# Performance work log

Measured on AMD Instinct MI355X. Metric: run time of the kernel, lower is better.

The kernel has to match this reference:

```python
import jax, jax.numpy as jnp
import numpy as np

TEMPERATURE = 0.07
TOP_MARGIN = 0.95
BOTTOM_MARGIN = 0.05

BATCH = 8192
DIM = 1024


def setup_inputs() -> dict:
    key = jax.random.key(0)
    kA, kB = jax.random.split(key)
    embedding_A = jax.random.normal(kA, (BATCH, DIM), dtype=jnp.float32)
    embedding_B = jax.random.normal(kB, (BATCH, DIM), dtype=jnp.float32)
    return {"embedding_A": embedding_A, "embedding_B": embedding_B}


def _l2norm(x):
    return x * jax.lax.rsqrt(jnp.sum(x * x, axis=-1, keepdims=True))


def reference(embedding_A, embedding_B):
    a = _l2norm(embedding_A)
    b = _l2norm(embedding_B)
    B = a.shape[0]
    sim = a @ b.T                                   # [B, B]
    pos = jnp.diagonal(sim)                         # [B]
    eye = jnp.eye(B, dtype=bool)
    upper = pos[:, None] * TOP_MARGIN
    lower = pos[:, None] * BOTTOM_MARGIN
    neg_mask = (sim <= upper) & (sim >= lower) & ~eye   # [B, B]

    # Per-row CE over [positive, hard negatives] == masked logsumexp - pos/tau.
    z = sim / TEMPERATURE
    full_mask = neg_mask | eye                      # positive always included
    masked = jnp.where(full_mask, z, -jnp.inf)
    m = jnp.max(masked, axis=1, keepdims=True)      # finite: diag always present
    lse = m[:, 0] + jnp.log(jnp.sum(jnp.exp(masked - m), axis=1))
    per_row = lse - pos / TEMPERATURE               # [B]

    valid = jnp.any(neg_mask, axis=1)               # rows with >=1 negative
    count = jnp.sum(valid)
    total = jnp.sum(jnp.where(valid, per_row, 0.0))
    return total / jnp.maximum(count, 1).astype(total.dtype)
```

## Files before the change

### kernel.cpp

```cpp
#include <hip/hip_runtime.h>
#include <hip/hip_bf16.h>

#define BATCH 8192
#define DIM   1024
#define INV_TAU (1.0f / 0.07f)
#define TOPM 0.95f
#define BOTM 0.05f

#define BM 256
#define BN 256
#define BK 64
#define NT (DIM / BK)

typedef __attribute__((ext_vector_type(4))) float f32x4;
typedef __attribute__((ext_vector_type(8))) short bf16x8;

typedef __attribute__((address_space(3))) void       lds_void_t;
typedef const __attribute__((address_space(1))) void gbl_void_t;

__device__ inline void async_copy16(const void* g, void* l) {
    __builtin_amdgcn_global_load_lds((gbl_void_t*)g, (lds_void_t*)l, 16, 0, 0);
}

__device__ inline unsigned short f2bf(float f) {
    __hip_bfloat16 h = __float2bfloat16(f);
    return *reinterpret_cast<unsigned short*>(&h);
}

__global__ __launch_bounds__(256) void prep_kernel(
    const float* __restrict__ A, const float* __restrict__ B,
    unsigned short* __restrict__ An, unsigned short* __restrict__ Bn,
    float* __restrict__ pos, float* __restrict__ S)
{
    int row = blockIdx.x;
    int t = threadIdx.x;
    const float4* a4 = (const float4*)(A + (size_t)row * DIM);
    const float4* b4 = (const float4*)(B + (size_t)row * DIM);
    float4 av = a4[t];
    float4 bv = b4[t];
    float sa = av.x*av.x + av.y*av.y + av.z*av.z + av.w*av.w;
    float sb = bv.x*bv.x + bv.y*bv.y + bv.z*bv.z + bv.w*bv.w;
    float dp = av.x*bv.x + av.y*bv.y + av.z*bv.z + av.w*bv.w;
    #pragma unroll
    for (int d = 32; d > 0; d >>= 1) {
        sa += __shfl_down(sa, d);
        sb += __shfl_down(sb, d);
        dp += __shfl_down(dp, d);
    }
    __shared__ float red[3][4];
    int lane = t & 63, w = t >> 6;
    if (lane == 0) { red[0][w] = sa; red[1][w] = sb; red[2][w] = dp; }
    __syncthreads();
    sa = red[0][0] + red[0][1] + red[0][2] + red[0][3];
    sb = red[1][0] + red[1][1] + red[1][2] + red[1][3];
    dp = red[2][0] + red[2][1] + red[2][2] + red[2][3];
    float ra = rsqrtf(sa);
    float rb = rsqrtf(sb);
    if (t == 0) {
        pos[row] = dp * ra * rb;
        S[row] = 0.0f;
    }
    ushort4 oa, ob;
    oa.x = f2bf(av.x * ra); oa.y = f2bf(av.y * ra);
    oa.z = f2bf(av.z * ra); oa.w = f2bf(av.w * ra);
    ob.x = f2bf(bv.x * rb); ob.y = f2bf(bv.y * rb);
    ob.z = f2bf(bv.z * rb); ob.w = f2bf(bv.w * rb);
    ((ushort4*)(An + (size_t)row * DIM))[t] = oa;
    ((ushort4*)(Bn + (size_t)row * DIM))[t] = ob;
}

__global__ __launch_bounds__(512, 2) void sim_loss_kernel(
    const unsigned short* __restrict__ An, const unsigned short* __restrict__ Bn,
    const float* __restrict__ pos, float* __restrict__ S)
{
    __shared__ char lds[131072];

    int tid  = threadIdx.x;
    int lane = tid & 63;
    int wave = tid >> 6;
    int wm = wave >> 2, wn = wave & 3;
    int fr = lane & 15;
    int q  = lane >> 4;

    int bid = blockIdx.x;

#define BASES(g, rB, cB) do {                                                        \
    int xcd_ = bid & 7, jj_ = bid >> 3;                                              \
    int qr_ = (g) >> 1, qc_ = ((g) & 1) ^ (qr_ & 1);                                 \
    (rB) = (qr_ * 16 + (xcd_ >> 1) * 4 + (jj_ >> 3)) * BM;                           \
    (cB) = (qc_ * 16 + (xcd_ & 1) * 8 + (jj_ & 7)) * BN;                             \
} while (0)

    f32x4 acc[8][4] = {};
    bf16x8 a0[4][2];
    bf16x8 a1[4][2];
    bf16x8 b0[2][2];
    bf16x8 b1[2][2];

    int sw = (fr & 7) << 4;
    int c0 = (q * 16) ^ sw;
    int c1 = (64 + q * 16) ^ sw;
    int aRow = (wm * 128 + fr) * 128;
    int bRow = (wn * 64 + fr) * 128;

    int strow = tid >> 3;
    int scb   = ((tid & 7) * 16) ^ ((strow & 7) << 4);
    int ldst = tid * 16;

#define PANELS(rB, cB, pA, pB) do {                                                  \
    (pA) = (const char*)An + (size_t)((rB) + strow) * 2048 + scb;                    \
    (pB) = (const char*)Bn + (size_t)((cB) + strow) * 2048 + scb;                    \
} while (0)

#define STAGE(gbase, u, h, ldsdst) do {                                              \
    async_copy16((gbase) + (size_t)(h) * 262144 + (size_t)(u) * 128,                 \
                 (ldsdst) + (h) * 16384 + ldst);                                     \
    async_copy16((gbase) + (size_t)(h) * 262144 + 131072 + (size_t)(u) * 128,        \
                 (ldsdst) + (h) * 16384 + 8192 + ldst);                              \
} while (0)

#define LDA_(arr, p, mh) do {                                                        \
    const char* _s = lds + (p) * 32768;                                              \
    _Pragma("unroll") for (int m = 0; m < 4; ++m) {                                  \
        arr[m][0] = *(const bf16x8*)(_s + aRow + (mh) * 8192 + m * 2048 + c0);       \
        arr[m][1] = *(const bf16x8*)(_s + aRow + (mh) * 8192 + m * 2048 + c1);       \
    }                                                                                \
} while (0)

#define LDB_(arr, p, nh) do {                                                        \
    const char* _s = lds + 65536 + (p) * 32768;                                      \
    _Pragma("unroll") for (int n = 0; n < 2; ++n) {                                  \
        arr[n][0] = *(const bf16x8*)(_s + bRow + (nh) * 4096 + n * 2048 + c0);       \
        arr[n][1] = *(const bf16x8*)(_s + bRow + (nh) * 4096 + n * 2048 + c1);       \
    }                                                                                \
} while (0)

#define MMA_(aarr, barr, mo, no) do {                                                \
    _Pragma("unroll") for (int m = 0; m < 4; ++m)                                    \
    _Pragma("unroll") for (int n = 0; n < 2; ++n) {                                  \
        acc[(mo)+m][(no)+n] = __builtin_amdgcn_mfma_f32_16x16x32_bf16(               \
            aarr[m][0], barr[n][0], acc[(mo)+m][(no)+n], 0, 0, 0);                   \
        acc[(mo)+m][(no)+n] = __builtin_amdgcn_mfma_f32_16x16x32_bf16(               \
            aarr[m][1], barr[n][1], acc[(mo)+m][(no)+n], 0, 0, 0);                   \
    }                                                                                \
} while (0)

#define BAR() __builtin_amdgcn_s_barrier()
#define SCH() __builtin_amdgcn_sched_barrier(0)
#define LGKM0() asm volatile("s_waitcnt lgkmcnt(0)" ::: "memory")
#define VMC(n)  asm volatile("s_waitcnt vmcnt(" #n ")" ::: "memory")
#define PRI1() __builtin_amdgcn_s_setprio(1)
#define PRI0() __builtin_amdgcn_s_setprio(0)

#define KTILE(p, pA_, uA, pB_, uB) do {                                              \
    char* stA = lds + (p) * 32768;                                                   \
    char* stB = lds + 65536 + (p) * 32768;                                           \
     BAR(); SCH();                                                           \
    LDA_(a0, (p), 0); LDB_(b0, (p), 0);                                              \
    PRI1(); MMA_(a0, b0, 0, 0); PRI0();                                              \
    LGKM0();                                                                         \
     BAR(); SCH();                                                           \
    LDA_(a1, (p), 1); LDB_(b1, (p), 1);                                              \
    PRI1(); MMA_(a0, b1, 0, 2); PRI0();                                              \
    LGKM0();                                                                         \
     BAR(); SCH();                                                           \
    STAGE((pA_), (uA), 0, stA); STAGE((pA_), (uA), 1, stA);                          \
    STAGE((pB_), (uB), 0, stB); STAGE((pB_), (uB), 1, stB);                          \
    PRI1(); MMA_(a1, b1, 4, 2); MMA_(a1, b0, 4, 0); PRI0();                          \
    VMC(8);                                                                          \
} while (0)

    int rowB, colB;
    BASES(0, rowB, colB);
    const char *gAc, *gBc;
    PANELS(rowB, colB, gAc, gBc);

    STAGE(gAc, 0, 0, lds);
    STAGE(gAc, 0, 1, lds);
    STAGE(gBc, 0, 0, lds + 65536);
    STAGE(gBc, 0, 1, lds + 65536);
    STAGE(gAc, 1, 0, lds + 32768);
    STAGE(gAc, 1, 1, lds + 32768);
    STAGE(gBc, 1, 0, lds + 98304);
    STAGE(gBc, 1, 1, lds + 98304);
    VMC(0);

    #pragma unroll 1
    for (int g = 0; g < 4; ++g) {
        int gn = (g < 3) ? g + 1 : 3;
        int rowBn, colBn;
        BASES(gn, rowBn, colBn);
        const char *gAn2, *gBn2;
        PANELS(rowBn, colBn, gAn2, gBn2);

        #pragma unroll 1
        for (int tt = 0; tt < 7; ++tt) {
            KTILE(0, gAc, 2 * tt + 2, gBc, 2 * tt + 2);
            KTILE(1, gAc, 2 * tt + 3, gBc, 2 * tt + 3);
        }
        KTILE(0, gAn2, 0, gBn2, 0);
        KTILE(1, gAn2, 1, gBn2, 1);

        #pragma unroll
        for (int m = 0; m < 8; ++m) {
            #pragma unroll
            for (int j2 = 0; j2 < 4; ++j2) {
                int i = rowB + wm * 128 + m * 16 + q * 4 + j2;
                float p  = pos[i];
                float up = TOPM * p, lo = BOTM * p;
                float rs = 0.0f;
                #pragma unroll
                for (int n = 0; n < 4; ++n) {
                    float sv = acc[m][n][j2];
                    int col = colB + wn * 64 + n * 16 + fr;
                    if (sv <= up && sv >= lo && col != i)
                        rs += __expf((sv - p) * INV_TAU);
                }
                #pragma unroll
                for (int d = 1; d < 16; d <<= 1)
                    rs += __shfl_xor(rs, d);
                if (fr == 0 && rs != 0.0f)
                    atomicAdd(&S[i], rs);
            }
        }
        #pragma unroll
        for (int m2 = 0; m2 < 8; ++m2)
            #pragma unroll
            for (int n2 = 0; n2 < 4; ++n2)
                acc[m2][n2] = (f32x4){0.0f, 0.0f, 0.0f, 0.0f};

        gAc = gAn2; gBc = gBn2; rowB = rowBn; colB = colBn;
    }
    LGKM0();
    VMC(0);

#undef BASES
#undef PANELS
#undef STAGE
#undef LDA_
#undef LDB_
#undef MMA_
#undef BAR
#undef SCH
#undef LGKM0
#undef VMC
#undef PRI1
#undef PRI0
#undef KTILE
}

__global__ __launch_bounds__(256) void finalize_kernel(
    const float* __restrict__ S, float* __restrict__ out)
{
    int t = threadIdx.x;
    float tot = 0.0f;
    int c = 0;
    for (int i = t; i < BATCH; i += 256) {
        float s = S[i];
        if (s > 0.0f) { tot += log1pf(s); c += 1; }
    }
    #pragma unroll
    for (int d = 32; d > 0; d >>= 1) {
        tot += __shfl_down(tot, d);
        c   += __shfl_down(c, d);
    }
    __shared__ float st[4];
    __shared__ int   sc[4];
    int lane = t & 63, w = t >> 6;
    if (lane == 0) { st[w] = tot; sc[w] = c; }
    __syncthreads();
    if (t == 0) {
        float T = st[0] + st[1] + st[2] + st[3];
        int   C = sc[0] + sc[1] + sc[2] + sc[3];
        out[0] = T / (float)(C > 0 ? C : 1);
    }
}

extern "C" void kernel_launch(void* const* d_in, const int* in_sizes, int n_in,
                              void* d_out, int out_size, void* d_ws, size_t ws_size,
                              hipStream_t stream) {
    const float* A = (const float*)d_in[0];
    const float* B = (const float*)d_in[1];

    char* ws = (char*)d_ws;
    unsigned short* An = (unsigned short*)ws;
    unsigned short* Bn = An + (size_t)BATCH * DIM;
    float* pos = (float*)(Bn + (size_t)BATCH * DIM);
    float* S   = pos + BATCH;
    float* out = (float*)d_out;

    prep_kernel<<<BATCH, 256, 0, stream>>>(A, B, An, Bn, pos, S);
    sim_loss_kernel<<<256, 512, 0, stream>>>(An, Bn, pos, S);
    finalize_kernel<<<1, 256, 0, stream>>>(S, out);
}
```

Measured before the change: 224.4 us.

## Replace hand-scheduled three-barrier K-tile pipeline with simple double-buffer prefetch

Replaces the fine-grained K-tile schedule with a simple one. The old schedule interleaved LDS reads and MFMAs across three barriers, with explicit waitcnt and sched_barrier control and two tiles prefetched. The new schedule issues the next tile's global-to-LDS copy into the other buffer, loads all fragments, runs all MFMAs, then does a single __syncthreads. It also changes launch bounds from 2 to 1 block per CU, which lets each thread use more registers but halves possible occupancy. The intent is to cut barrier and wait overhead, at the risk of less overlap between memory and compute and fewer waves to hide latency.

```diff
diff --git a/kernel.cpp b/kernel.cpp
--- a/kernel.cpp
+++ b/kernel.cpp
@@ -69,7 +69,7 @@
     ((ushort4*)(Bn + (size_t)row * DIM))[t] = ob;
 }
 
-__global__ __launch_bounds__(512, 2) void sim_loss_kernel(
+__global__ __launch_bounds__(512, 1) void sim_loss_kernel(
     const unsigned short* __restrict__ An, const unsigned short* __restrict__ Bn,
     const float* __restrict__ pos, float* __restrict__ S)
 {
@@ -145,29 +145,19 @@
     }                                                                                \
 } while (0)
 
-#define BAR() __builtin_amdgcn_s_barrier()
-#define SCH() __builtin_amdgcn_sched_barrier(0)
-#define LGKM0() asm volatile("s_waitcnt lgkmcnt(0)" ::: "memory")
-#define VMC(n)  asm volatile("s_waitcnt vmcnt(" #n ")" ::: "memory")
 #define PRI1() __builtin_amdgcn_s_setprio(1)
 #define PRI0() __builtin_amdgcn_s_setprio(0)
 
 #define KTILE(p, pA_, uA, pB_, uB) do {                                              \
-    char* stA = lds + (p) * 32768;                                                   \
-    char* stB = lds + 65536 + (p) * 32768;                                           \
-     BAR(); SCH();                                                           \
-    LDA_(a0, (p), 0); LDB_(b0, (p), 0);                                              \
-    PRI1(); MMA_(a0, b0, 0, 0); PRI0();                                              \
-    LGKM0();                                                                         \
-     BAR(); SCH();                                                           \
-    LDA_(a1, (p), 1); LDB_(b1, (p), 1);                                              \
-    PRI1(); MMA_(a0, b1, 0, 2); PRI0();                                              \
-    LGKM0();                                                                         \
-     BAR(); SCH();                                                           \
+    char* stA = lds + ((p) ^ 1) * 32768;                                             \
+    char* stB = lds + 65536 + ((p) ^ 1) * 32768;                                     \
     STAGE((pA_), (uA), 0, stA); STAGE((pA_), (uA), 1, stA);                          \
     STAGE((pB_), (uB), 0, stB); STAGE((pB_), (uB), 1, stB);                          \
-    PRI1(); MMA_(a1, b1, 4, 2); MMA_(a1, b0, 4, 0); PRI0();                          \
-    VMC(8);                                                                          \
+    LDA_(a0, (p), 0); LDA_(a1, (p), 1); LDB_(b0, (p), 0); LDB_(b1, (p), 1);          \
+    PRI1();                                                                          \
+    MMA_(a0, b0, 0, 0); MMA_(a0, b1, 0, 2); MMA_(a1, b1, 4, 2); MMA_(a1, b0, 4, 0);  \
+    PRI0();                                                                          \
+    __syncthreads();                                                                 \
 } while (0)
 
     int rowB, colB;
@@ -179,11 +169,7 @@
     STAGE(gAc, 0, 1, lds);
     STAGE(gBc, 0, 0, lds + 65536);
     STAGE(gBc, 0, 1, lds + 65536);
-    STAGE(gAc, 1, 0, lds + 32768);
-    STAGE(gAc, 1, 1, lds + 32768);
-    STAGE(gBc, 1, 0, lds + 98304);
-    STAGE(gBc, 1, 1, lds + 98304);
-    VMC(0);
+    __syncthreads();
 
     #pragma unroll 1
     for (int g = 0; g < 4; ++g) {
@@ -195,11 +181,11 @@
 
         #pragma unroll 1
         for (int tt = 0; tt < 7; ++tt) {
-            KTILE(0, gAc, 2 * tt + 2, gBc, 2 * tt + 2);
-            KTILE(1, gAc, 2 * tt + 3, gBc, 2 * tt + 3);
+            KTILE(0, gAc, 2 * tt + 1, gBc, 2 * tt + 1);
+            KTILE(1, gAc, 2 * tt + 2, gBc, 2 * tt + 2);
         }
-        KTILE(0, gAn2, 0, gBn2, 0);
-        KTILE(1, gAn2, 1, gBn2, 1);
+        KTILE(0, gAc, 15, gBc, 15);
+        KTILE(1, gAn2, 0, gBn2, 0);
 
         #pragma unroll
         for (int m = 0; m < 8; ++m) {
@@ -231,8 +217,6 @@
 
         gAc = gAn2; gBc = gBn2; rowB = rowBn; colB = colBn;
     }
-    LGKM0();
-    VMC(0);
 
 #undef BASES
 #undef PANELS
@@ -240,10 +224,6 @@
 #undef LDA_
 #undef LDB_
 #undef MMA_
-#undef BAR
-#undef SCH
-#undef LGKM0
-#undef VMC
 #undef PRI1
 #undef PRI0
 #undef KTILE
```

Result: faster. 214.3 us (-4.5%).
